# Kernel tuning notes

Hardware: AMD Instinct MI355X
Metric: run time of the kernel (lower is better)

## Reference

```python
import jax, jax.numpy as jnp
import numpy as np

N = 50000      # nodes
E = 1600000    # edges
L = 128        # latent_size


def _mlp(h, W1, b1, W2, b2):
    # MLP(in_dim, [L, L]) == Linear -> ReLU -> Linear
    return jax.nn.relu(h @ W1 + b1) @ W2 + b2


def setup_inputs() -> dict:
    key = jax.random.key(0)
    ks = jax.random.split(key, 12)
    glorot = lambda k, i, o: jax.random.normal(k, (i, o), jnp.float32) * (2.0 / (i + o)) ** 0.5
    return {
        "pos": jax.random.normal(ks[0], (N, 3), jnp.float32),
        "x": jax.random.normal(ks[1], (N, L), jnp.float32),
        "edge_attr": jax.random.normal(ks[2], (E, L), jnp.float32),
        "edge_index": jax.random.randint(ks[3], (2, E), 0, N, jnp.int64),
        "last_pred": jax.random.normal(ks[4], (N, 3), jnp.float32),
        "mask_idx": jax.random.randint(ks[5], (N, 1), 0, 2, jnp.int32).astype(bool),
        # pos_embedding MLP params (in=3)
        "Wp1": glorot(ks[6], 3, L), "bp1": jnp.zeros((L,), jnp.float32),
        "Wp2": glorot(ks[7], L, L), "bp2": jnp.zeros((L,), jnp.float32),
        # dis_embedding MLP params (in=1)
        "Wd1": glorot(ks[8], 1, L), "bd1": jnp.zeros((L,), jnp.float32),
        "Wd2": glorot(ks[9], L, L), "bd2": jnp.zeros((L,), jnp.float32),
    }


def reference(pos, x, edge_attr, edge_index, last_pred, mask_idx,
              Wp1, bp1, Wp2, bp2, Wd1, bd1, Wd2, bd2):
    # mode == 'mask': replace masked node positions with last prediction
    pos = jnp.where(mask_idx, last_pred, pos)                    # [N,3]
    extended_x = x + _mlp(pos, Wp1, bp1, Wp2, bp2)               # [N,L]
    row, col = edge_index[0], edge_index[1]
    diff = pos[row] - pos[col]                                   # [E,3]
    length = jnp.linalg.norm(diff, axis=-1, keepdims=True)       # [E,1]
    extended_edge_attr = edge_attr + _mlp(length, Wd1, bd1, Wd2, bd2)  # [E,L]
    return extended_x, extended_edge_attr
```

## Files before the change

### kernel.cpp

```cpp
#include <hip/hip_runtime.h>
#include <hip/hip_bf16.h>

#define NN 50000
#define EE 1600000
#define NT_N 391
#define NIV 129

typedef float f32x4 __attribute__((ext_vector_type(4)));
typedef __bf16 bf16x8 __attribute__((ext_vector_type(8)));

__device__ float gT[128];
__device__ int   gRank[128];
__device__ __align__(16) float gA[NIV * 128];
__device__ __align__(16) float gB[NIV * 128];

__device__ __forceinline__ float edge_len(int e, const int* __restrict__ eidx,
                                          const float* __restrict__ pos,
                                          const float* __restrict__ lp,
                                          const int* __restrict__ msk) {
    int ri = eidx[e];
    int ci = eidx[EE + e];
    const float* pr = msk[ri] ? lp : pos;
    const float* pc = msk[ci] ? lp : pos;
    float dx = pr[3 * ri + 0] - pc[3 * ci + 0];
    float dy = pr[3 * ri + 1] - pc[3 * ci + 1];
    float dz = pr[3 * ri + 2] - pc[3 * ci + 2];
    return sqrtf(dx * dx + dy * dy + dz * dz);
}

__global__ void prep1(const float* __restrict__ Wd1, const float* __restrict__ bd1) {
    int k = threadIdx.x;
    float w1 = Wd1[k], b1 = bd1[k];
    float t = (w1 == 0.f) ? __builtin_inff() : (-b1 / w1);
    int rank = 0;
    for (int j = 0; j < 128; j++) {
        float w1j = Wd1[j], b1j = bd1[j];
        float tj = (w1j == 0.f) ? __builtin_inff() : (-b1j / w1j);
        rank += (tj < t) || (tj == t && j < k);
    }
    gRank[k] = rank;
    gT[rank] = t;
}

__global__ void prep2(const float* __restrict__ Wd1, const float* __restrict__ bd1,
                      const float* __restrict__ Wd2, const float* __restrict__ bd2) {
    int i = blockIdx.x;
    int c = threadIdx.x;
    float a = 0.f, b = 0.f;
    for (int k = 0; k < 128; k++) {
        float w1 = Wd1[k], b1 = bd1[k];
        bool act = (w1 > 0.f) ? (gRank[k] < i)
                 : (w1 < 0.f) ? (gRank[k] >= i)
                              : (b1 > 0.f);
        if (act) {
            float w2 = Wd2[k * 128 + c];
            a = fmaf(w1, w2, a);
            b = fmaf(b1, w2, b);
        }
    }
    gA[i * 128 + c] = a;
    gB[i * 128 + c] = b + bd2[c];
}

__global__ __launch_bounds__(256) void len_kernel(
    const int* __restrict__ eidx, const float* __restrict__ pos,
    const float* __restrict__ lp, const int* __restrict__ msk,
    float* __restrict__ len)
{
    int e = blockIdx.x * 256 + threadIdx.x;
    if (e < EE) len[e] = edge_len(e, eidx, pos, lp, msk);
}

template <bool PRECOMP>
__global__ __launch_bounds__(256) void edge_kernel(
    const float* __restrict__ ea, const float* __restrict__ len,
    const int* __restrict__ eidx, const float* __restrict__ pos,
    const float* __restrict__ lp, const int* __restrict__ msk,
    float* __restrict__ oute)
{
    __shared__ float ts[128];
    if (threadIdx.x < 128) ts[threadIdx.x] = gT[threadIdx.x];
    __syncthreads();

    const int g  = threadIdx.x >> 5;
    const int c4 = (threadIdx.x & 31) * 4;

    for (int r = blockIdx.x * 8 + g; r < EE; r += gridDim.x * 8) {
        float lv = PRECOMP ? len[r] : edge_len(r, eidx, pos, lp, msk);

        int lo = 0;
#pragma unroll
        for (int s = 128; s > 0; s >>= 1) {
            int m = lo + s;
            if (m <= 128 && ts[m - 1] < lv) lo = m;
        }

        const f32x4 a = *(const f32x4*)&gA[lo * 128 + c4];
        const f32x4 b = *(const f32x4*)&gB[lo * 128 + c4];
        const size_t off = (size_t)r * 128 + c4;
        f32x4 e = __builtin_nontemporal_load((const f32x4*)(ea + off));
        f32x4 o = e + (lv * a + b);
        __builtin_nontemporal_store(o, (f32x4*)(oute + off));
    }
}

__device__ __forceinline__ void stage_w2(const float* __restrict__ W2, __bf16* w2l) {
    for (int idx = threadIdx.x; idx < 128 * 128; idx += 512) {
        int k = idx >> 7;
        int c = idx & 127;
        int dst = (((k >> 5) * 8 + (c >> 4)) * 64 + (((k >> 3) & 3) * 16 + (c & 15))) * 8 + (k & 7);
        w2l[dst] = (__bf16)W2[idx];
    }
}

__global__ __launch_bounds__(512, 3) void node_kernel(
    const float* __restrict__ pos, const float* __restrict__ x,
    const float* __restrict__ lp, const int* __restrict__ msk,
    const float* __restrict__ Wp1, const float* __restrict__ bp1,
    const float* __restrict__ Wp2, const float* __restrict__ bp2,
    float* __restrict__ outx)
{
    __shared__ __bf16 w2l[16384];
    __shared__ float w1l[384], b1l[128], b2l[128];
    __shared__ float tbuf[8][512];

    stage_w2(Wp2, w2l);
    for (int i = threadIdx.x; i < 384; i += 512) w1l[i] = Wp1[i];
    if (threadIdx.x < 128) {
        b1l[threadIdx.x] = bp1[threadIdx.x];
        b2l[threadIdx.x] = bp2[threadIdx.x];
    }
    __syncthreads();

    const int w = threadIdx.x >> 6;
    const int l = threadIdx.x & 63;
    const int llo = l & 15;
    const int lgrp = l >> 4;
    float* tb = tbuf[w];

    const int base = blockIdx.x * 128;
    const int e0 = base + w * 16;
    const bool valid = (e0 + 16 <= NN);

    f32x4 ear[8];
    f32x4 acc[8];
    if (valid) {
        const float* srow = x + (size_t)e0 * 128;
#pragma unroll
        for (int j = 0; j < 8; j++) ear[j] = *(const f32x4*)(srow + j * 256 + l * 4);

        int nd = e0 + llo;
        const float* p = msk[nd] ? lp : pos;
        float px = p[3 * nd + 0];
        float py = p[3 * nd + 1];
        float pz = p[3 * nd + 2];

#pragma unroll
        for (int m = 0; m < 8; m++) acc[m] = (f32x4){0.f, 0.f, 0.f, 0.f};

#pragma unroll
        for (int kk = 0; kk < 4; kk++) {
            bf16x8 hf;
#pragma unroll
            for (int j = 0; j < 8; j++) {
                int k = kk * 32 + lgrp * 8 + j;
                float h = px * w1l[k] + py * w1l[128 + k] + pz * w1l[256 + k] + b1l[k];
                hf[j] = (__bf16)fmaxf(h, 0.f);
            }
#pragma unroll
            for (int m = 0; m < 8; m++) {
                bf16x8 wf = *(const bf16x8*)&w2l[((kk * 8 + m) * 64 + l) * 8];
                acc[m] = __builtin_amdgcn_mfma_f32_16x16x32_bf16(wf, hf, acc[m], 0, 0, 0);
            }
        }
    }

    float* drow = outx + (size_t)e0 * 128;
    f32x4 b2v = *(const f32x4*)&b2l[(l & 31) * 4];

#pragma unroll
    for (int p = 0; p < 4; p++) {
        if (valid && (llo >> 2) == p) {
            int r = llo & 3;
#pragma unroll
            for (int m = 0; m < 8; m++) {
                int c = (m * 16 + lgrp * 4 + r * 4) & 127;
                *(f32x4*)&tb[r * 128 + c] = acc[m];
            }
        }
        __syncthreads();
        if (valid) {
#pragma unroll
            for (int i = 0; i < 2; i++) {
                int row = 2 * i + (l >> 5);
                int c = ((l & 31) * 4 + row * 4) & 127;
                f32x4 tv = *(const f32x4*)&tb[row * 128 + c];
                f32x4 o = tv + b2v + ear[p * 2 + i];
                *(f32x4*)(drow + p * 512 + i * 256 + l * 4) = o;
            }
        }
        __syncthreads();
    }
}

extern "C" void kernel_launch(void* const* d_in, const int* in_sizes, int n_in,
                              void* d_out, int out_size, void* d_ws, size_t ws_size,
                              hipStream_t stream) {
    const float* pos        = (const float*)d_in[0];
    const float* x          = (const float*)d_in[1];
    const float* edge_attr  = (const float*)d_in[2];
    const int* edge_index   = (const int*)d_in[3];
    const float* last_pred  = (const float*)d_in[4];
    const int* mask         = (const int*)d_in[5];
    const float* Wp1 = (const float*)d_in[6];
    const float* bp1 = (const float*)d_in[7];
    const float* Wp2 = (const float*)d_in[8];
    const float* bp2 = (const float*)d_in[9];
    const float* Wd1 = (const float*)d_in[10];
    const float* bd1 = (const float*)d_in[11];
    const float* Wd2 = (const float*)d_in[12];
    const float* bd2 = (const float*)d_in[13];

    float* outx = (float*)d_out;
    float* oute = outx + (size_t)NN * 128;
    float* len  = (float*)d_ws;

    prep1<<<1, 128, 0, stream>>>(Wd1, bd1);
    prep2<<<NIV, 128, 0, stream>>>(Wd1, bd1, Wd2, bd2);

    node_kernel<<<NT_N, 512, 0, stream>>>(pos, x, last_pred, mask,
                                          Wp1, bp1, Wp2, bp2, outx);

    if (ws_size >= (size_t)EE * sizeof(float)) {
        len_kernel<<<(EE + 255) / 256, 256, 0, stream>>>(edge_index, pos, last_pred, mask, len);
        edge_kernel<true><<<2048, 256, 0, stream>>>(edge_attr, len, edge_index,
                                                    pos, last_pred, mask, oute);
    } else {
        edge_kernel<false><<<2048, 256, 0, stream>>>(edge_attr, nullptr, edge_index,
                                                     pos, last_pred, mask, oute);
    }
}
```

Before: 383.2 us.

## Merge prep kernels, precompute interval index with edge length, process two edges per group

Fuses the two table-building kernels into one, which recomputes the rank in shared memory in every block, and drops one launch. The length kernel now also does the binary search over breakpoints and stores a (length, interval) pair, so the main edge kernel reads these pairs and skips the per-row search. The edge kernel now handles two rows per 32-lane group per iteration to raise memory-level parallelism. The trade-off is twice the workspace traffic for the length/interval pairs, plus redundant rank computation across blocks.

Measured after the change: 385.9 us. Within noise of the previous version (+0.7%).

```diff
diff --git a/kernel.cpp b/kernel.cpp
--- a/kernel.cpp
+++ b/kernel.cpp
@@ -10,7 +10,6 @@
 typedef __bf16 bf16x8 __attribute__((ext_vector_type(8)));
 
 __device__ float gT[128];
-__device__ int   gRank[128];
 __device__ __align__(16) float gA[NIV * 128];
 __device__ __align__(16) float gB[NIV * 128];
 
@@ -28,79 +27,118 @@
     return sqrtf(dx * dx + dy * dy + dz * dz);
 }
 
-__global__ void prep1(const float* __restrict__ Wd1, const float* __restrict__ bd1) {
-    int k = threadIdx.x;
-    float w1 = Wd1[k], b1 = bd1[k];
+__global__ void prep_tables(const float* __restrict__ Wd1, const float* __restrict__ bd1,
+                            const float* __restrict__ Wd2, const float* __restrict__ bd2) {
+    __shared__ float t_s[128];
+    __shared__ int rank_s[128];
+    const int c = threadIdx.x;
+    float w1 = Wd1[c], b1 = bd1[c];
     float t = (w1 == 0.f) ? __builtin_inff() : (-b1 / w1);
+    t_s[c] = t;
+    __syncthreads();
     int rank = 0;
     for (int j = 0; j < 128; j++) {
-        float w1j = Wd1[j], b1j = bd1[j];
-        float tj = (w1j == 0.f) ? __builtin_inff() : (-b1j / w1j);
-        rank += (tj < t) || (tj == t && j < k);
-    }
-    gRank[k] = rank;
-    gT[rank] = t;
-}
-
-__global__ void prep2(const float* __restrict__ Wd1, const float* __restrict__ bd1,
-                      const float* __restrict__ Wd2, const float* __restrict__ bd2) {
-    int i = blockIdx.x;
-    int c = threadIdx.x;
+        float tj = t_s[j];
+        rank += (tj < t) || (tj == t && j < c);
+    }
+    rank_s[c] = rank;
+    if (blockIdx.x == 0) gT[rank] = t;
+    __syncthreads();
+
+    const int i = blockIdx.x;
     float a = 0.f, b = 0.f;
     for (int k = 0; k < 128; k++) {
-        float w1 = Wd1[k], b1 = bd1[k];
-        bool act = (w1 > 0.f) ? (gRank[k] < i)
-                 : (w1 < 0.f) ? (gRank[k] >= i)
-                              : (b1 > 0.f);
+        float w1k = Wd1[k], b1k = bd1[k];
+        bool act = (w1k > 0.f) ? (rank_s[k] < i)
+                 : (w1k < 0.f) ? (rank_s[k] >= i)
+                               : (b1k > 0.f);
         if (act) {
             float w2 = Wd2[k * 128 + c];
-            a = fmaf(w1, w2, a);
-            b = fmaf(b1, w2, b);
+            a = fmaf(w1k, w2, a);
+            b = fmaf(b1k, w2, b);
         }
     }
     gA[i * 128 + c] = a;
     gB[i * 128 + c] = b + bd2[c];
 }
 
-__global__ __launch_bounds__(256) void len_kernel(
+__global__ __launch_bounds__(256) void leniv_kernel(
     const int* __restrict__ eidx, const float* __restrict__ pos,
     const float* __restrict__ lp, const int* __restrict__ msk,
-    float* __restrict__ len)
-{
-    int e = blockIdx.x * 256 + threadIdx.x;
-    if (e < EE) len[e] = edge_len(e, eidx, pos, lp, msk);
-}
-
-template <bool PRECOMP>
-__global__ __launch_bounds__(256) void edge_kernel(
-    const float* __restrict__ ea, const float* __restrict__ len,
-    const int* __restrict__ eidx, const float* __restrict__ pos,
-    const float* __restrict__ lp, const int* __restrict__ msk,
-    float* __restrict__ oute)
+    float2* __restrict__ lenivp)
 {
     __shared__ float ts[128];
     if (threadIdx.x < 128) ts[threadIdx.x] = gT[threadIdx.x];
     __syncthreads();
-
-    const int g  = threadIdx.x >> 5;
-    const int c4 = (threadIdx.x & 31) * 4;
-
-    for (int r = blockIdx.x * 8 + g; r < EE; r += gridDim.x * 8) {
-        float lv = PRECOMP ? len[r] : edge_len(r, eidx, pos, lp, msk);
-
+    int e = blockIdx.x * 256 + threadIdx.x;
+    if (e < EE) {
+        float lv = edge_len(e, eidx, pos, lp, msk);
         int lo = 0;
 #pragma unroll
         for (int s = 128; s > 0; s >>= 1) {
             int m = lo + s;
             if (m <= 128 && ts[m - 1] < lv) lo = m;
         }
-
-        const f32x4 a = *(const f32x4*)&gA[lo * 128 + c4];
-        const f32x4 b = *(const f32x4*)&gB[lo * 128 + c4];
-        const size_t off = (size_t)r * 128 + c4;
-        f32x4 e = __builtin_nontemporal_load((const f32x4*)(ea + off));
-        f32x4 o = e + (lv * a + b);
-        __builtin_nontemporal_store(o, (f32x4*)(oute + off));
+        lenivp[e] = make_float2(lv, (float)lo);
+    }
+}
+
+__global__ __launch_bounds__(256) void len_kernel(
+    const int* __restrict__ eidx, const float* __restrict__ pos,
+    const float* __restrict__ lp, const int* __restrict__ msk,
+    float* __restrict__ len)
+{
+    int e = blockIdx.x * 256 + threadIdx.x;
+    if (e < EE) len[e] = edge_len(e, eidx, pos, lp, msk);
+}
+
+template <int MODE>
+__global__ __launch_bounds__(256) void edge_kernel(
+    const float* __restrict__ ea, const float2* __restrict__ lenivp,
+    const float* __restrict__ len,
+    const int* __restrict__ eidx, const float* __restrict__ pos,
+    const float* __restrict__ lp, const int* __restrict__ msk,
+    float* __restrict__ oute)
+{
+    __shared__ float ts[128];
+    if (MODE != 0) {
+        if (threadIdx.x < 128) ts[threadIdx.x] = gT[threadIdx.x];
+        __syncthreads();
+    }
+
+    const int g  = threadIdx.x >> 5;
+    const int c4 = (threadIdx.x & 31) * 4;
+
+    for (int r0 = (blockIdx.x * 8 + g) * 2; r0 < EE; r0 += gridDim.x * 16) {
+        float len0, len1;
+        int iv0, iv1;
+        if (MODE == 0) {
+            f32x4 lv = *(const f32x4*)&lenivp[r0];
+            len0 = lv.x; iv0 = (int)lv.y;
+            len1 = lv.z; iv1 = (int)lv.w;
+        } else {
+            len0 = (MODE == 1) ? len[r0]     : edge_len(r0, eidx, pos, lp, msk);
+            len1 = (MODE == 1) ? len[r0 + 1] : edge_len(r0 + 1, eidx, pos, lp, msk);
+            iv0 = 0; iv1 = 0;
+#pragma unroll
+            for (int s = 128; s > 0; s >>= 1) {
+                int m0 = iv0 + s;
+                if (m0 <= 128 && ts[m0 - 1] < len0) iv0 = m0;
+                int m1 = iv1 + s;
+                if (m1 <= 128 && ts[m1 - 1] < len1) iv1 = m1;
+            }
+        }
+
+        const f32x4 a0 = *(const f32x4*)&gA[iv0 * 128 + c4];
+        const f32x4 b0 = *(const f32x4*)&gB[iv0 * 128 + c4];
+        const f32x4 a1 = *(const f32x4*)&gA[iv1 * 128 + c4];
+        const f32x4 b1 = *(const f32x4*)&gB[iv1 * 128 + c4];
+
+        const size_t off0 = (size_t)r0 * 128 + c4;
+        f32x4 e0 = __builtin_nontemporal_load((const f32x4*)(ea + off0));
+        f32x4 e1 = __builtin_nontemporal_load((const f32x4*)(ea + off0 + 128));
+        __builtin_nontemporal_store(e0 + (len0 * a0 + b0), (f32x4*)(oute + off0));
+        __builtin_nontemporal_store(e1 + (len1 * a1 + b1), (f32x4*)(oute + off0 + 128));
     }
 }
 
@@ -223,20 +261,26 @@
 
     float* outx = (float*)d_out;
     float* oute = outx + (size_t)NN * 128;
-    float* len  = (float*)d_ws;
-
-    prep1<<<1, 128, 0, stream>>>(Wd1, bd1);
-    prep2<<<NIV, 128, 0, stream>>>(Wd1, bd1, Wd2, bd2);
+
+    prep_tables<<<NIV, 128, 0, stream>>>(Wd1, bd1, Wd2, bd2);
 
     node_kernel<<<NT_N, 512, 0, stream>>>(pos, x, last_pred, mask,
                                           Wp1, bp1, Wp2, bp2, outx);
 
-    if (ws_size >= (size_t)EE * sizeof(float)) {
-        len_kernel<<<(EE + 255) / 256, 256, 0, stream>>>(edge_index, pos, last_pred, mask, len);
-        edge_kernel<true><<<2048, 256, 0, stream>>>(edge_attr, len, edge_index,
-                                                    pos, last_pred, mask, oute);
+    if (ws_size >= (size_t)EE * 8) {
+        float2* lenivp = (float2*)d_ws;
+        leniv_kernel<<<(EE + 255) / 256, 256, 0, stream>>>(
+            edge_index, pos, last_pred, mask, lenivp);
+        edge_kernel<0><<<2048, 256, 0, stream>>>(
+            edge_attr, lenivp, nullptr, edge_index, pos, last_pred, mask, oute);
+    } else if (ws_size >= (size_t)EE * 4) {
+        float* len = (float*)d_ws;
+        len_kernel<<<(EE + 255) / 256, 256, 0, stream>>>(
+            edge_index, pos, last_pred, mask, len);
+        edge_kernel<1><<<2048, 256, 0, stream>>>(
+            edge_attr, nullptr, len, edge_index, pos, last_pred, mask, oute);
     } else {
-        edge_kernel<false><<<2048, 256, 0, stream>>>(edge_attr, nullptr, edge_index,
-                                                     pos, last_pred, mask, oute);
-    }
-}
+        edge_kernel<2><<<2048, 256, 0, stream>>>(
+            edge_attr, nullptr, nullptr, edge_index, pos, last_pred, mask, oute);
+    }
+}
```

## Fuse prep into node kernel and inline edge length into batched edge kernel

Applied to the files above, without the earlier changes.

Merges the two piecewise-linear table prep kernels into extra blocks of the node MLP kernel, using a shared-memory union. It also removes the separate edge-length pass and workspace round trip by computing lengths inline. The edge kernel now handles four rows per group, issuing their loads together to expose more memory-level parallelism. Edge-attribute loads and output stores switch from nontemporal to plain accesses, which may change cache behaviour on the large streaming traffic.

Measured after the change: 379.9 us. About the same (-0.9%).

```diff
diff --git a/kernel.cpp b/kernel.cpp
--- a/kernel.cpp
+++ b/kernel.cpp
@@ -3,14 +3,13 @@
 
 #define NN 50000
 #define EE 1600000
-#define NT_N 391
+#define NB_NODE 391
 #define NIV 129
 
 typedef float f32x4 __attribute__((ext_vector_type(4)));
 typedef __bf16 bf16x8 __attribute__((ext_vector_type(8)));
 
 __device__ float gT[128];
-__device__ int   gRank[128];
 __device__ __align__(16) float gA[NIV * 128];
 __device__ __align__(16) float gB[NIV * 128];
 
@@ -28,81 +27,18 @@
     return sqrtf(dx * dx + dy * dy + dz * dz);
 }
 
-__global__ void prep1(const float* __restrict__ Wd1, const float* __restrict__ bd1) {
-    int k = threadIdx.x;
-    float w1 = Wd1[k], b1 = bd1[k];
-    float t = (w1 == 0.f) ? __builtin_inff() : (-b1 / w1);
-    int rank = 0;
-    for (int j = 0; j < 128; j++) {
-        float w1j = Wd1[j], b1j = bd1[j];
-        float tj = (w1j == 0.f) ? __builtin_inff() : (-b1j / w1j);
-        rank += (tj < t) || (tj == t && j < k);
-    }
-    gRank[k] = rank;
-    gT[rank] = t;
-}
-
-__global__ void prep2(const float* __restrict__ Wd1, const float* __restrict__ bd1,
-                      const float* __restrict__ Wd2, const float* __restrict__ bd2) {
-    int i = blockIdx.x;
-    int c = threadIdx.x;
-    float a = 0.f, b = 0.f;
-    for (int k = 0; k < 128; k++) {
-        float w1 = Wd1[k], b1 = bd1[k];
-        bool act = (w1 > 0.f) ? (gRank[k] < i)
-                 : (w1 < 0.f) ? (gRank[k] >= i)
-                              : (b1 > 0.f);
-        if (act) {
-            float w2 = Wd2[k * 128 + c];
-            a = fmaf(w1, w2, a);
-            b = fmaf(b1, w2, b);
-        }
-    }
-    gA[i * 128 + c] = a;
-    gB[i * 128 + c] = b + bd2[c];
-}
-
-__global__ __launch_bounds__(256) void len_kernel(
-    const int* __restrict__ eidx, const float* __restrict__ pos,
-    const float* __restrict__ lp, const int* __restrict__ msk,
-    float* __restrict__ len)
-{
-    int e = blockIdx.x * 256 + threadIdx.x;
-    if (e < EE) len[e] = edge_len(e, eidx, pos, lp, msk);
-}
-
-template <bool PRECOMP>
-__global__ __launch_bounds__(256) void edge_kernel(
-    const float* __restrict__ ea, const float* __restrict__ len,
-    const int* __restrict__ eidx, const float* __restrict__ pos,
-    const float* __restrict__ lp, const int* __restrict__ msk,
-    float* __restrict__ oute)
-{
-    __shared__ float ts[128];
-    if (threadIdx.x < 128) ts[threadIdx.x] = gT[threadIdx.x];
-    __syncthreads();
-
-    const int g  = threadIdx.x >> 5;
-    const int c4 = (threadIdx.x & 31) * 4;
-
-    for (int r = blockIdx.x * 8 + g; r < EE; r += gridDim.x * 8) {
-        float lv = PRECOMP ? len[r] : edge_len(r, eidx, pos, lp, msk);
-
-        int lo = 0;
-#pragma unroll
-        for (int s = 128; s > 0; s >>= 1) {
-            int m = lo + s;
-            if (m <= 128 && ts[m - 1] < lv) lo = m;
-        }
-
-        const f32x4 a = *(const f32x4*)&gA[lo * 128 + c4];
-        const f32x4 b = *(const f32x4*)&gB[lo * 128 + c4];
-        const size_t off = (size_t)r * 128 + c4;
-        f32x4 e = __builtin_nontemporal_load((const f32x4*)(ea + off));
-        f32x4 o = e + (lv * a + b);
-        __builtin_nontemporal_store(o, (f32x4*)(oute + off));
-    }
-}
+union SM {
+    struct {
+        __bf16 w2l[16384];
+        float w1l[384], b1l[128], b2l[128];
+        float tbuf[8][512];
+    } n;
+    struct {
+        float t_s[128];
+        int   rank_s[128];
+        float pa[4][128], pb[4][128];
+    } p;
+};
 
 __device__ __forceinline__ void stage_w2(const float* __restrict__ W2, __bf16* w2l) {
     for (int idx = threadIdx.x; idx < 128 * 128; idx += 512) {
@@ -113,22 +49,67 @@
     }
 }
 
-__global__ __launch_bounds__(512, 3) void node_kernel(
+__global__ __launch_bounds__(512, 3) void node_prep_kernel(
     const float* __restrict__ pos, const float* __restrict__ x,
     const float* __restrict__ lp, const int* __restrict__ msk,
     const float* __restrict__ Wp1, const float* __restrict__ bp1,
     const float* __restrict__ Wp2, const float* __restrict__ bp2,
+    const float* __restrict__ Wd1, const float* __restrict__ bd1,
+    const float* __restrict__ Wd2, const float* __restrict__ bd2,
     float* __restrict__ outx)
 {
-    __shared__ __bf16 w2l[16384];
-    __shared__ float w1l[384], b1l[128], b2l[128];
-    __shared__ float tbuf[8][512];
-
-    stage_w2(Wp2, w2l);
-    for (int i = threadIdx.x; i < 384; i += 512) w1l[i] = Wp1[i];
+    __shared__ SM sm;
+
+    if (blockIdx.x >= NB_NODE) {
+        const int i = blockIdx.x - NB_NODE;
+        const int c = threadIdx.x & 127;
+        const int q = threadIdx.x >> 7;
+        if (q == 0) {
+            float w1 = Wd1[c], b1 = bd1[c];
+            sm.p.t_s[c] = (w1 == 0.f) ? __builtin_inff() : (-b1 / w1);
+        }
+        __syncthreads();
+        if (q == 0) {
+            float t = sm.p.t_s[c];
+            int rank = 0;
+            for (int j = 0; j < 128; j++) {
+                float tj = sm.p.t_s[j];
+                rank += (tj < t) || (tj == t && j < c);
+            }
+            sm.p.rank_s[c] = rank;
+            if (i == 0) gT[rank] = t;
+        }
+        __syncthreads();
+        float a = 0.f, b = 0.f;
+        for (int kk = 0; kk < 32; kk++) {
+            int k = q * 32 + kk;
+            float w1k = Wd1[k], b1k = bd1[k];
+            bool act = (w1k > 0.f) ? (sm.p.rank_s[k] < i)
+                     : (w1k < 0.f) ? (sm.p.rank_s[k] >= i)
+                                   : (b1k > 0.f);
+            if (act) {
+                float w2 = Wd2[k * 128 + c];
+                a = fmaf(w1k, w2, a);
+                b = fmaf(b1k, w2, b);
+            }
+        }
+        sm.p.pa[q][c] = a;
+        sm.p.pb[q][c] = b;
+        __syncthreads();
+        if (q == 0) {
+            float A = sm.p.pa[0][c] + sm.p.pa[1][c] + sm.p.pa[2][c] + sm.p.pa[3][c];
+            float B = sm.p.pb[0][c] + sm.p.pb[1][c] + sm.p.pb[2][c] + sm.p.pb[3][c];
+            gA[i * 128 + c] = A;
+            gB[i * 128 + c] = B + bd2[c];
+        }
+        return;
+    }
+
+    stage_w2(Wp2, sm.n.w2l);
+    for (int i = threadIdx.x; i < 384; i += 512) sm.n.w1l[i] = Wp1[i];
     if (threadIdx.x < 128) {
-        b1l[threadIdx.x] = bp1[threadIdx.x];
-        b2l[threadIdx.x] = bp2[threadIdx.x];
+        sm.n.b1l[threadIdx.x] = bp1[threadIdx.x];
+        sm.n.b2l[threadIdx.x] = bp2[threadIdx.x];
     }
     __syncthreads();
 
@@ -136,10 +117,9 @@
     const int l = threadIdx.x & 63;
     const int llo = l & 15;
     const int lgrp = l >> 4;
-    float* tb = tbuf[w];
-
-    const int base = blockIdx.x * 128;
-    const int e0 = base + w * 16;
+    float* tb = sm.n.tbuf[w];
+
+    const int e0 = blockIdx.x * 128 + w * 16;
     const bool valid = (e0 + 16 <= NN);
 
     f32x4 ear[8];
@@ -164,19 +144,20 @@
 #pragma unroll
             for (int j = 0; j < 8; j++) {
                 int k = kk * 32 + lgrp * 8 + j;
-                float h = px * w1l[k] + py * w1l[128 + k] + pz * w1l[256 + k] + b1l[k];
+                float h = px * sm.n.w1l[k] + py * sm.n.w1l[128 + k]
+                        + pz * sm.n.w1l[256 + k] + sm.n.b1l[k];
                 hf[j] = (__bf16)fmaxf(h, 0.f);
             }
 #pragma unroll
             for (int m = 0; m < 8; m++) {
-                bf16x8 wf = *(const bf16x8*)&w2l[((kk * 8 + m) * 64 + l) * 8];
+                bf16x8 wf = *(const bf16x8*)&sm.n.w2l[((kk * 8 + m) * 64 + l) * 8];
                 acc[m] = __builtin_amdgcn_mfma_f32_16x16x32_bf16(wf, hf, acc[m], 0, 0, 0);
             }
         }
     }
 
     float* drow = outx + (size_t)e0 * 128;
-    f32x4 b2v = *(const f32x4*)&b2l[(l & 31) * 4];
+    f32x4 b2v = *(const f32x4*)&sm.n.b2l[(l & 31) * 4];
 
 #pragma unroll
     for (int p = 0; p < 4; p++) {
@@ -200,6 +181,47 @@
             }
         }
         __syncthreads();
+    }
+}
+
+__global__ __launch_bounds__(256) void edge_kernel(
+    const float* __restrict__ ea, const int* __restrict__ eidx,
+    const float* __restrict__ pos, const float* __restrict__ lp,
+    const int* __restrict__ msk, float* __restrict__ oute)
+{
+    __shared__ float ts[128];
+    if (threadIdx.x < 128) ts[threadIdx.x] = gT[threadIdx.x];
+    __syncthreads();
+
+    const int g  = threadIdx.x >> 5;
+    const int c4 = (threadIdx.x & 31) * 4;
+
+    for (int r0 = (blockIdx.x * 8 + g) * 4; r0 < EE; r0 += gridDim.x * 32) {
+        f32x4 e[4];
+#pragma unroll
+        for (int j = 0; j < 4; j++)
+            e[j] = *(const f32x4*)(ea + (size_t)(r0 + j) * 128 + c4);
+
+        float lenv[4];
+        int iv[4];
+#pragma unroll
+        for (int j = 0; j < 4; j++) {
+            lenv[j] = edge_len(r0 + j, eidx, pos, lp, msk);
+            int lo = 0;
+#pragma unroll
+            for (int s = 128; s > 0; s >>= 1) {
+                int m = lo + s;
+                if (m <= 128 && ts[m - 1] < lenv[j]) lo = m;
+            }
+            iv[j] = lo;
+        }
+
+#pragma unroll
+        for (int j = 0; j < 4; j++) {
+            const f32x4 a = *(const f32x4*)&gA[iv[j] * 128 + c4];
+            const f32x4 b = *(const f32x4*)&gB[iv[j] * 128 + c4];
+            *(f32x4*)(oute + (size_t)(r0 + j) * 128 + c4) = e[j] + (lenv[j] * a + b);
+        }
     }
 }
 
@@ -223,20 +245,11 @@
 
     float* outx = (float*)d_out;
     float* oute = outx + (size_t)NN * 128;
-    float* len  = (float*)d_ws;
-
-    prep1<<<1, 128, 0, stream>>>(Wd1, bd1);
-    prep2<<<NIV, 128, 0, stream>>>(Wd1, bd1, Wd2, bd2);
-
-    node_kernel<<<NT_N, 512, 0, stream>>>(pos, x, last_pred, mask,
-                                          Wp1, bp1, Wp2, bp2, outx);
-
-    if (ws_size >= (size_t)EE * sizeof(float)) {
-        len_kernel<<<(EE + 255) / 256, 256, 0, stream>>>(edge_index, pos, last_pred, mask, len);
-        edge_kernel<true><<<2048, 256, 0, stream>>>(edge_attr, len, edge_index,
-                                                    pos, last_pred, mask, oute);
-    } else {
-        edge_kernel<false><<<2048, 256, 0, stream>>>(edge_attr, nullptr, edge_index,
-                                                     pos, last_pred, mask, oute);
-    }
-}
+
+    node_prep_kernel<<<NB_NODE + NIV, 512, 0, stream>>>(
+        pos, x, last_pred, mask,
+        Wp1, bp1, Wp2, bp2, Wd1, bd1, Wd2, bd2, outx);
+
+    edge_kernel<<<2048, 256, 0, stream>>>(
+        edge_attr, edge_index, pos, last_pred, mask, oute);
+}
```
